# Kernel tuning notes

Hardware: AMD Instinct MI355X
Metric: run time of the kernel (lower is better)

The kernel has to match this reference:

```python
import jax, jax.numpy as jnp
import numpy as np

B, N, M = 8, 4096, 4096


def setup_inputs() -> dict:
    key = jax.random.key(0)
    ks = jax.random.split(key, 8)
    return {
        "x_aligned": jax.random.normal(ks[0], (B, N, 3), dtype=jnp.float32),
        "y": jax.random.normal(ks[1], (B, M, 3), dtype=jnp.float32),
        "R": jax.random.normal(ks[2], (B, 3, 3), dtype=jnp.float32),
        "S": jax.random.normal(ks[3], (B, 3), dtype=jnp.float32),
        "t": jax.random.normal(ks[4], (B, 3, 1), dtype=jnp.float32),
        "R_gt": jax.random.normal(ks[5], (B, 3, 3), dtype=jnp.float32),
        "S_gt": jax.random.normal(ks[6], (B, 3), dtype=jnp.float32),
        "t_gt": jax.random.normal(ks[7], (B, 3), dtype=jnp.float32),
    }


def chamfer_distance(x, y):
    # x: [B,N,3], y: [B,M,3]; bidirectional mean squared NN distance
    xn = jnp.sum(x * x, axis=-1)                      # [B,N]
    yn = jnp.sum(y * y, axis=-1)                      # [B,M]
    xy = jnp.einsum('bnd,bmd->bnm', x, y)             # [B,N,M]
    d2 = xn[:, :, None] + yn[:, None, :] - 2.0 * xy   # [B,N,M] squared dists
    cham_x = jnp.mean(jnp.min(d2, axis=2), axis=1)    # [B] x -> y
    cham_y = jnp.mean(jnp.min(d2, axis=1), axis=1)    # [B] y -> x
    return jnp.mean(cham_x) + jnp.mean(cham_y)        # batch mean, summed dirs


def reference(x_aligned, y, R, S, t, R_gt, S_gt, t_gt):
    t = jnp.squeeze(t)                                # [B,3]
    eye = jnp.eye(3, dtype=R.dtype)
    R_loss = jnp.einsum('bij,bkj->bik', R, R_gt) - eye  # R @ R_gt^T - I
    L_reg = (jnp.sum(R_loss * R_loss)
             + jnp.sum((S - S_gt) ** 2)
             + jnp.sum((t - t_gt) ** 2))
    L_chamfer = chamfer_distance(x_aligned, y)
    return L_reg + L_chamfer
```

## Files before the change

kernel.cpp:

```cpp
#include <hip/hip_runtime.h>

#define BB 8
#define NN 4096
#define NZB 16
#define MC 256
#define NCHUNK (NN / MC)
#define TPB 256
#define NPTS (NZB * NN)

typedef short short8 __attribute__((ext_vector_type(8)));
typedef float f32x4 __attribute__((ext_vector_type(4)));

#define APACK_SHORTS (NZB * NCHUNK * 8192)
#define BPACK_SHORTS (NZB * NN * 32)

__device__ __forceinline__ unsigned short b16(float v) {
  const unsigned u = __float_as_uint(v);
  return (unsigned short)((u + 0x7fffu + ((u >> 16) & 1u)) >> 16);
}
__device__ __forceinline__ float fb16(unsigned short h) {
  return __uint_as_float(((unsigned)h) << 16);
}
__device__ __forceinline__ void split3(float v, unsigned short* o) {
  const unsigned short h0 = b16(v); const float f0 = fb16(h0);
  const unsigned short h1 = b16(v - f0); const float f1 = fb16(h1);
  const unsigned short h2 = b16(v - f0 - f1);
  o[0] = h0; o[1] = h1; o[2] = h2;
}

__global__ __launch_bounds__(TPB) void hegn_prep(
    const float* __restrict__ X, const float* __restrict__ Y,
    unsigned short* __restrict__ Apack, unsigned short* __restrict__ Bpack,
    float* __restrict__ qn, float* __restrict__ out) {
  const int id = blockIdx.x * TPB + threadIdx.x;
  if (id == 0) *out = 0.0f;
  const int role = id >> 16;
  const int zb = (id >> 12) & 15;
  const int j = id & (NN - 1);
  const int b = zb & 7;
  const int dir = zb >> 3;
  const float* src = (role == 0) ? (dir ? X + b * NN * 3 : Y + b * NN * 3)
                                 : (dir ? Y + b * NN * 3 : X + b * NN * 3);
  const float a0 = src[j * 3 + 0];
  const float a1 = src[j * 3 + 1];
  const float a2 = src[j * 3 + 2];
  unsigned short s0[3], s1[3], s2[3];
  if (role == 0) {
    split3(a0, s0); split3(a1, s1); split3(a2, s2);
    const float n = fmaf(a0, a0, fmaf(a1, a1, a2 * a2));
    unsigned short n3[3]; split3(n, n3);
    unsigned short* dst = Apack + (zb * NCHUNK + (j >> 8)) * 8192 +
                          (((j >> 4) & 15) * 64 + (j & 15)) * 8;
    const unsigned short* r[3] = {s0, s1, s2};
#pragma unroll
    for (int d = 0; d < 3; d++) {
      short8 w;
      w[0] = r[d][0]; w[1] = r[d][0]; w[2] = r[d][1]; w[3] = r[d][1];
      w[4] = r[d][0]; w[5] = r[d][2]; w[6] = r[d][1]; w[7] = r[d][2];
      *(short8*)(dst + d * 128) = w;
    }
    short8 w;
    w[0] = n3[0]; w[1] = n3[1]; w[2] = n3[2];
    w[3] = 0; w[4] = 0; w[5] = 0; w[6] = 0; w[7] = 0;
    *(short8*)(dst + 3 * 128) = w;
  } else {
    split3(-2.0f * a0, s0); split3(-2.0f * a1, s1); split3(-2.0f * a2, s2);
    unsigned short* dst = Bpack + (zb * NN + j) * 32;
    const unsigned short* s[3] = {s0, s1, s2};
#pragma unroll
    for (int d = 0; d < 3; d++) {
      short8 w;
      w[0] = s[d][0]; w[1] = s[d][1]; w[2] = s[d][0]; w[3] = s[d][1];
      w[4] = s[d][2]; w[5] = s[d][0]; w[6] = s[d][2]; w[7] = s[d][1];
      *(short8*)(dst + d * 8) = w;
    }
    short8 w;
    w[0] = (short)0x3f80; w[1] = (short)0x3f80; w[2] = (short)0x3f80;
    w[3] = 0; w[4] = 0; w[5] = 0; w[6] = 0; w[7] = 0;
    *(short8*)(dst + 24) = w;
    qn[zb * NN + j] = fmaf(a0, a0, fmaf(a1, a1, a2 * a2));
  }
}

__global__ __launch_bounds__(TPB) void hegn_chamfer(
    const unsigned short* __restrict__ Apack,
    const unsigned short* __restrict__ Bpack,
    const float* __restrict__ qn, float* __restrict__ partial) {
  __shared__ short8 As[1024];
  const int tid = threadIdx.x;
  const int zb = blockIdx.z;
  const int c  = blockIdx.y;
  const int l  = tid & 63;
  const int wid = tid >> 6;
  const int wavebase = blockIdx.x * 512 + wid * 128;

  {
    const float4* src = (const float4*)(Apack + (zb * NCHUNK + c) * 8192);
    float4* dst = (float4*)As;
#pragma unroll
    for (int i = 0; i < 4; i++) dst[i * TPB + tid] = src[i * TPB + tid];
  }

  const int col = l & 15, kb = l >> 4;
  short8 Bf[8]; float qf[8];
#pragma unroll
  for (int f = 0; f < 8; f++) {
    const int q = wavebase + f * 16 + col;
    Bf[f] = *(const short8*)(Bpack + (zb * NN + q) * 32 + kb * 8);
    qf[f] = qn[zb * NN + q];
  }
  float m[8];
#pragma unroll
  for (int f = 0; f < 8; f++) m[f] = 1e30f;
  const f32x4 Z = {0.0f, 0.0f, 0.0f, 0.0f};
  __syncthreads();

#pragma unroll 2
  for (int tt = 0; tt < 16; tt++) {
    const short8 A = As[tt * 64 + l];
#pragma unroll
    for (int f = 0; f < 8; f++) {
      const f32x4 D = __builtin_amdgcn_mfma_f32_16x16x32_bf16(A, Bf[f], Z, 0, 0, 0);
      m[f] = fminf(m[f], fminf(fminf(D[0], D[1]), fminf(D[2], D[3])));
    }
  }

#pragma unroll
  for (int f = 0; f < 8; f++) {
    float v = m[f];
    v = fminf(v, __shfl_xor(v, 16));
    v = fminf(v, __shfl_xor(v, 32));
    m[f] = v + qf[f];
  }
  const int g = l >> 4;
  const float v1 = g == 0 ? m[0] : g == 1 ? m[1] : g == 2 ? m[2] : m[3];
  const float v2 = g == 0 ? m[4] : g == 1 ? m[5] : g == 2 ? m[6] : m[7];
  float* pp = partial + (c * NZB + zb) * NN + wavebase;
  pp[l] = v1;
  pp[64 + l] = v2;
}

__global__ __launch_bounds__(256) void chamfer_reduce(
    const float4* __restrict__ partial4,
    const float* __restrict__ R, const float* __restrict__ S,
    const float* __restrict__ t, const float* __restrict__ Rgt,
    const float* __restrict__ Sgt, const float* __restrict__ tgt,
    float* __restrict__ out) {
  const int tid = threadIdx.x;
  const int q4 = blockIdx.x * 256 + tid;
  float4 mn = make_float4(1e30f, 1e30f, 1e30f, 1e30f);
#pragma unroll
  for (int c = 0; c < NCHUNK; c++) {
    const float4 v = partial4[c * (NPTS / 4) + q4];
    mn.x = fminf(mn.x, v.x);
    mn.y = fminf(mn.y, v.y);
    mn.z = fminf(mn.z, v.z);
    mn.w = fminf(mn.w, v.w);
  }
  float s = (mn.x + mn.y) + (mn.z + mn.w);
  for (int o = 32; o > 0; o >>= 1) s += __shfl_down(s, o);
  __shared__ float wsum[4];
  if ((tid & 63) == 0) wsum[tid >> 6] = s;
  __syncthreads();
  if (tid == 0) {
    const float bs = wsum[0] + wsum[1] + wsum[2] + wsum[3];
    atomicAdd(out, bs * (1.0f / (float)(BB * NN)));
  }

  if (blockIdx.x == 0) {
    float v = 0.0f;
    if (tid < 72) {
      const int b = tid / 9, ik = tid % 9, i = ik / 3, k = ik % 3;
      const float* Rb = R + b * 9;
      const float* Gb = Rgt + b * 9;
      float d = Rb[i * 3 + 0] * Gb[k * 3 + 0] +
                Rb[i * 3 + 1] * Gb[k * 3 + 1] +
                Rb[i * 3 + 2] * Gb[k * 3 + 2];
      d -= (i == k) ? 1.0f : 0.0f;
      v = d * d;
    } else if (tid < 96) {
      const int i = tid - 72;
      const float d = S[i] - Sgt[i];
      v = d * d;
    } else if (tid < 120) {
      const int i = tid - 96;
      const float d = t[i] - tgt[i];
      v = d * d;
    }
    for (int o = 32; o > 0; o >>= 1) v += __shfl_down(v, o);
    __shared__ float rsum[4];
    if ((tid & 63) == 0) rsum[tid >> 6] = v;
    __syncthreads();
    if (tid == 0) atomicAdd(out, rsum[0] + rsum[1] + rsum[2] + rsum[3]);
  }
}

extern "C" void kernel_launch(void* const* d_in, const int* in_sizes, int n_in,
                              void* d_out, int out_size, void* d_ws, size_t ws_size,
                              hipStream_t stream) {
  const float* X   = (const float*)d_in[0];
  const float* Y   = (const float*)d_in[1];
  const float* R   = (const float*)d_in[2];
  const float* S   = (const float*)d_in[3];
  const float* t   = (const float*)d_in[4];
  const float* Rgt = (const float*)d_in[5];
  const float* Sgt = (const float*)d_in[6];
  const float* tgt = (const float*)d_in[7];

  unsigned short* Apack = (unsigned short*)d_ws;
  unsigned short* Bpack = Apack + APACK_SHORTS;
  float* qn       = (float*)(Bpack + BPACK_SHORTS);
  float* partial  = qn + NPTS;
  float* out      = (float*)d_out;

  hegn_prep<<<2 * NZB * NN / TPB, TPB, 0, stream>>>(X, Y, Apack, Bpack, qn, out);

  dim3 gC(8, NCHUNK, NZB);
  hegn_chamfer<<<gC, TPB, 0, stream>>>(Apack, Bpack, qn, partial);

  chamfer_reduce<<<NPTS / 4 / 256, 256, 0, stream>>>(
      (const float4*)partial, R, S, t, Rgt, Sgt, tgt, out);
}
```

Before: 102.6 us.

## Fuse bf16 split packing into chamfer kernel and process several chunks per block

Removes the separate prep kernel. The chamfer kernel now builds the 3-way bf16 split fragments and squared norms directly from X/Y: query fragments go into registers, and reference chunks go into shared memory. Each block loops over 4 reference chunks, which cuts the grid from 2048 to 512 blocks and the partial-min buffer from 16 chunks to 4. This saves one launch and the global round trip of the packed A/B/qn workspace. In exchange, split conversion work is repeated per block, an extra sync pair is added per chunk, and fewer blocks are available to fill the device.

```diff
diff --git a/kernel.cpp b/kernel.cpp
--- a/kernel.cpp
+++ b/kernel.cpp
@@ -4,15 +4,13 @@
 #define NN 4096
 #define NZB 16
 #define MC 256
-#define NCHUNK (NN / MC)
+#define CPG 4
+#define NCGRP 4
 #define TPB 256
 #define NPTS (NZB * NN)
 
 typedef short short8 __attribute__((ext_vector_type(8)));
 typedef float f32x4 __attribute__((ext_vector_type(4)));
-
-#define APACK_SHORTS (NZB * NCHUNK * 8192)
-#define BPACK_SHORTS (NZB * NN * 32)
 
 __device__ __forceinline__ unsigned short b16(float v) {
   const unsigned u = __float_as_uint(v);
@@ -28,100 +26,89 @@
   o[0] = h0; o[1] = h1; o[2] = h2;
 }
 
-__global__ __launch_bounds__(TPB) void hegn_prep(
+
+__global__ __launch_bounds__(TPB) void hegn_chamfer(
     const float* __restrict__ X, const float* __restrict__ Y,
-    unsigned short* __restrict__ Apack, unsigned short* __restrict__ Bpack,
-    float* __restrict__ qn, float* __restrict__ out) {
-  const int id = blockIdx.x * TPB + threadIdx.x;
-  if (id == 0) *out = 0.0f;
-  const int role = id >> 16;
-  const int zb = (id >> 12) & 15;
-  const int j = id & (NN - 1);
-  const int b = zb & 7;
-  const int dir = zb >> 3;
-  const float* src = (role == 0) ? (dir ? X + b * NN * 3 : Y + b * NN * 3)
-                                 : (dir ? Y + b * NN * 3 : X + b * NN * 3);
-  const float a0 = src[j * 3 + 0];
-  const float a1 = src[j * 3 + 1];
-  const float a2 = src[j * 3 + 2];
-  unsigned short s0[3], s1[3], s2[3];
-  if (role == 0) {
-    split3(a0, s0); split3(a1, s1); split3(a2, s2);
-    const float n = fmaf(a0, a0, fmaf(a1, a1, a2 * a2));
-    unsigned short n3[3]; split3(n, n3);
-    unsigned short* dst = Apack + (zb * NCHUNK + (j >> 8)) * 8192 +
-                          (((j >> 4) & 15) * 64 + (j & 15)) * 8;
-    const unsigned short* r[3] = {s0, s1, s2};
-#pragma unroll
-    for (int d = 0; d < 3; d++) {
-      short8 w;
-      w[0] = r[d][0]; w[1] = r[d][0]; w[2] = r[d][1]; w[3] = r[d][1];
-      w[4] = r[d][0]; w[5] = r[d][2]; w[6] = r[d][1]; w[7] = r[d][2];
-      *(short8*)(dst + d * 128) = w;
-    }
-    short8 w;
-    w[0] = n3[0]; w[1] = n3[1]; w[2] = n3[2];
-    w[3] = 0; w[4] = 0; w[5] = 0; w[6] = 0; w[7] = 0;
-    *(short8*)(dst + 3 * 128) = w;
-  } else {
-    split3(-2.0f * a0, s0); split3(-2.0f * a1, s1); split3(-2.0f * a2, s2);
-    unsigned short* dst = Bpack + (zb * NN + j) * 32;
-    const unsigned short* s[3] = {s0, s1, s2};
-#pragma unroll
-    for (int d = 0; d < 3; d++) {
-      short8 w;
-      w[0] = s[d][0]; w[1] = s[d][1]; w[2] = s[d][0]; w[3] = s[d][1];
-      w[4] = s[d][2]; w[5] = s[d][0]; w[6] = s[d][2]; w[7] = s[d][1];
-      *(short8*)(dst + d * 8) = w;
-    }
-    short8 w;
-    w[0] = (short)0x3f80; w[1] = (short)0x3f80; w[2] = (short)0x3f80;
-    w[3] = 0; w[4] = 0; w[5] = 0; w[6] = 0; w[7] = 0;
-    *(short8*)(dst + 24) = w;
-    qn[zb * NN + j] = fmaf(a0, a0, fmaf(a1, a1, a2 * a2));
-  }
-}
-
-__global__ __launch_bounds__(TPB) void hegn_chamfer(
-    const unsigned short* __restrict__ Apack,
-    const unsigned short* __restrict__ Bpack,
-    const float* __restrict__ qn, float* __restrict__ partial) {
+    float* __restrict__ partial, float* __restrict__ out) {
   __shared__ short8 As[1024];
   const int tid = threadIdx.x;
-  const int zb = blockIdx.z;
-  const int c  = blockIdx.y;
-  const int l  = tid & 63;
+  const int zb  = blockIdx.z;
+  const int cg  = blockIdx.y;
+  const int b   = zb & (BB - 1);
+  const int dir = zb >> 3;
+  const float* qsrc = dir ? (Y + b * NN * 3) : (X + b * NN * 3);
+  const float* rsrc = dir ? (X + b * NN * 3) : (Y + b * NN * 3);
+  const int l   = tid & 63;
   const int wid = tid >> 6;
   const int wavebase = blockIdx.x * 512 + wid * 128;
 
-  {
-    const float4* src = (const float4*)(Apack + (zb * NCHUNK + c) * 8192);
-    float4* dst = (float4*)As;
-#pragma unroll
-    for (int i = 0; i < 4; i++) dst[i * TPB + tid] = src[i * TPB + tid];
-  }
+  if (tid == 0 && blockIdx.x == 0 && blockIdx.y == 0 && blockIdx.z == 0)
+    *out = 0.0f;
 
   const int col = l & 15, kb = l >> 4;
-  short8 Bf[8]; float qf[8];
+  short8 Bf[8]; float qf[8]; float m[8];
 #pragma unroll
   for (int f = 0; f < 8; f++) {
     const int q = wavebase + f * 16 + col;
-    Bf[f] = *(const short8*)(Bpack + (zb * NN + q) * 32 + kb * 8);
-    qf[f] = qn[zb * NN + q];
-  }
-  float m[8];
-#pragma unroll
-  for (int f = 0; f < 8; f++) m[f] = 1e30f;
+    const float a0 = qsrc[q * 3 + 0];
+    const float a1 = qsrc[q * 3 + 1];
+    const float a2 = qsrc[q * 3 + 2];
+    qf[f] = fmaf(a0, a0, fmaf(a1, a1, a2 * a2));
+    short8 w;
+    if (kb < 3) {
+      const float ad = (kb == 0) ? a0 : (kb == 1) ? a1 : a2;
+      unsigned short s[3]; split3(-2.0f * ad, s);
+      w[0] = s[0]; w[1] = s[1]; w[2] = s[0]; w[3] = s[1];
+      w[4] = s[2]; w[5] = s[0]; w[6] = s[2]; w[7] = s[1];
+    } else {
+      w[0] = (short)0x3f80; w[1] = (short)0x3f80; w[2] = (short)0x3f80;
+      w[3] = 0; w[4] = 0; w[5] = 0; w[6] = 0; w[7] = 0;
+    }
+    Bf[f] = w;
+    m[f] = 1e30f;
+  }
+
   const f32x4 Z = {0.0f, 0.0f, 0.0f, 0.0f};
-  __syncthreads();
+
+#pragma unroll 1
+  for (int i = 0; i < CPG; i++) {
+    const int cbase = (cg * CPG + i) * MC;
+    __syncthreads();
+    {
+      const int j = cbase + tid;
+      const float a0 = rsrc[j * 3 + 0];
+      const float a1 = rsrc[j * 3 + 1];
+      const float a2 = rsrc[j * 3 + 2];
+      unsigned short s0[3], s1[3], s2[3], n3[3];
+      split3(a0, s0); split3(a1, s1); split3(a2, s2);
+      const float n = fmaf(a0, a0, fmaf(a1, a1, a2 * a2));
+      split3(n, n3);
+      const int tt = tid >> 4, row = tid & 15;
+      short8* dst = &As[tt * 64 + row];
+      const unsigned short* r[3] = {s0, s1, s2};
+#pragma unroll
+      for (int d = 0; d < 3; d++) {
+        short8 w;
+        w[0] = r[d][0]; w[1] = r[d][0]; w[2] = r[d][1]; w[3] = r[d][1];
+        w[4] = r[d][0]; w[5] = r[d][2]; w[6] = r[d][1]; w[7] = r[d][2];
+        dst[d * 16] = w;
+      }
+      short8 w;
+      w[0] = n3[0]; w[1] = n3[1]; w[2] = n3[2];
+      w[3] = 0; w[4] = 0; w[5] = 0; w[6] = 0; w[7] = 0;
+      dst[3 * 16] = w;
+    }
+    __syncthreads();
 
 #pragma unroll 2
-  for (int tt = 0; tt < 16; tt++) {
-    const short8 A = As[tt * 64 + l];
-#pragma unroll
-    for (int f = 0; f < 8; f++) {
-      const f32x4 D = __builtin_amdgcn_mfma_f32_16x16x32_bf16(A, Bf[f], Z, 0, 0, 0);
-      m[f] = fminf(m[f], fminf(fminf(D[0], D[1]), fminf(D[2], D[3])));
+    for (int tt = 0; tt < 16; tt++) {
+      const short8 A = As[tt * 64 + l];
+#pragma unroll
+      for (int f = 0; f < 8; f++) {
+        const f32x4 D =
+            __builtin_amdgcn_mfma_f32_16x16x32_bf16(A, Bf[f], Z, 0, 0, 0);
+        m[f] = fminf(m[f], fminf(fminf(D[0], D[1]), fminf(D[2], D[3])));
+      }
     }
   }
 
@@ -135,7 +122,7 @@
   const int g = l >> 4;
   const float v1 = g == 0 ? m[0] : g == 1 ? m[1] : g == 2 ? m[2] : m[3];
   const float v2 = g == 0 ? m[4] : g == 1 ? m[5] : g == 2 ? m[6] : m[7];
-  float* pp = partial + (c * NZB + zb) * NN + wavebase;
+  float* pp = partial + (cg * NZB + zb) * NN + wavebase;
   pp[l] = v1;
   pp[64 + l] = v2;
 }
@@ -150,7 +137,7 @@
   const int q4 = blockIdx.x * 256 + tid;
   float4 mn = make_float4(1e30f, 1e30f, 1e30f, 1e30f);
 #pragma unroll
-  for (int c = 0; c < NCHUNK; c++) {
+  for (int c = 0; c < NCGRP; c++) {
     const float4 v = partial4[c * (NPTS / 4) + q4];
     mn.x = fminf(mn.x, v.x);
     mn.y = fminf(mn.y, v.y);
@@ -207,16 +194,11 @@
   const float* Sgt = (const float*)d_in[6];
   const float* tgt = (const float*)d_in[7];
 
-  unsigned short* Apack = (unsigned short*)d_ws;
-  unsigned short* Bpack = Apack + APACK_SHORTS;
-  float* qn       = (float*)(Bpack + BPACK_SHORTS);
-  float* partial  = qn + NPTS;
-  float* out      = (float*)d_out;
-
-  hegn_prep<<<2 * NZB * NN / TPB, TPB, 0, stream>>>(X, Y, Apack, Bpack, qn, out);
-
-  dim3 gC(8, NCHUNK, NZB);
-  hegn_chamfer<<<gC, TPB, 0, stream>>>(Apack, Bpack, qn, partial);
+  float* partial = (float*)d_ws;
+  float* out     = (float*)d_out;
+
+  dim3 gC(8, NCGRP, NZB);
+  hegn_chamfer<<<gC, TPB, 0, stream>>>(X, Y, partial, out);
 
   chamfer_reduce<<<NPTS / 4 / 256, 256, 0, stream>>>(
       (const float4*)partial, R, S, t, Rgt, Sgt, tgt, out);
```

New measurement: 97.62 us. 1.05x faster.
